# Kernel tuning notes

Measured on AMD Instinct MI355X. Metric: run time of the kernel, lower is better.

## Reference

```python
import jax, jax.numpy as jnp
import numpy as np

N_NODES = 50000
N_EDGES = 1600000
N_GRAPHS = 2048
DIM = 133
EPS = 1e-5


def gcn_conv(x, W, b, row, col, n_nodes):
    # PyG GCNConv: h = x @ W; add self-loops; sym-normalized scatter-add; + b
    h = x @ W  # [N, D]
    loops = jnp.arange(n_nodes, dtype=row.dtype)
    r = jnp.concatenate([row, loops])
    c = jnp.concatenate([col, loops])
    deg = jax.ops.segment_sum(jnp.ones_like(c, dtype=h.dtype), c, num_segments=n_nodes)
    dinv = jnp.where(deg > 0, jax.lax.rsqrt(deg), 0.0)
    norm = dinv[r] * dinv[c]  # [E+N]
    msg = h[r] * norm[:, None]  # gather + scale
    out = jax.ops.segment_sum(msg, c, num_segments=n_nodes)
    return out + b


def batchnorm_eval(x, gamma, beta, rm, rv):
    return (x - rm) * jax.lax.rsqrt(rv + EPS) * gamma + beta


def setup_inputs() -> dict:
    key = jax.random.key(0)
    ks = jax.random.split(key, 8)
    x = jax.random.normal(ks[0], (N_NODES, DIM), dtype=jnp.float32)
    edge_index = jax.random.randint(ks[1], (2, N_EDGES), 0, N_NODES, dtype=jnp.int64)
    batch = jnp.sort(jax.random.randint(ks[2], (N_NODES,), 0, N_GRAPHS, dtype=jnp.int64))
    s = 1.0 / np.sqrt(DIM)
    W1 = jax.random.uniform(ks[3], (DIM, DIM), jnp.float32, -s, s)
    W2 = jax.random.uniform(ks[4], (DIM, DIM), jnp.float32, -s, s)
    b1 = jnp.zeros((DIM,), jnp.float32)
    b2 = jnp.zeros((DIM,), jnp.float32)
    g1 = jnp.ones((DIM,), jnp.float32); beta1 = jnp.zeros((DIM,), jnp.float32)
    rm1 = jax.random.normal(ks[5], (DIM,), jnp.float32) * 0.1
    rv1 = jnp.ones((DIM,), jnp.float32)
    g2 = jnp.ones((DIM,), jnp.float32); beta2 = jnp.zeros((DIM,), jnp.float32)
    rm2 = jax.random.normal(ks[6], (DIM,), jnp.float32) * 0.1
    rv2 = jnp.ones((DIM,), jnp.float32)
    return {"x": x, "edge_index": edge_index, "batch": batch,
            "W1": W1, "b1": b1, "W2": W2, "b2": b2,
            "g1": g1, "beta1": beta1, "rm1": rm1, "rv1": rv1,
            "g2": g2, "beta2": beta2, "rm2": rm2, "rv2": rv2}


def reference(x, edge_index, batch, W1, b1, W2, b2,
              g1, beta1, rm1, rv1, g2, beta2, rm2, rv2):
    row, col = edge_index[0], edge_index[1]
    h = gcn_conv(x, W1, b1, row, col, N_NODES)
    h = jax.nn.relu(h)
    h = batchnorm_eval(h, g1, beta1, rm1, rv1)  # eval-mode BN; dropout is identity in eval
    h = gcn_conv(h, W2, b2, row, col, N_NODES)
    h = jax.nn.relu(h)
    h = batchnorm_eval(h, g2, beta2, rm2, rv2)
    # global mean pool per graph
    sums = jax.ops.segment_sum(h, batch, num_segments=N_GRAPHS)
    cnts = jax.ops.segment_sum(jnp.ones((N_NODES,), h.dtype), batch, num_segments=N_GRAPHS)
    return sums / jnp.maximum(cnts, 1.0)[:, None]
```

## Files before the change

### kernel.cpp

```cpp
#include <hip/hip_runtime.h>

#define N_NODES  50000
#define N_ROWS   50048
#define N_EDGES  1600000
#define N_GRAPHS 2048
#define DIM      133
#define HSTR     136
#define YSTR     160
#define EPSV     1e-5f
#define NRANGE   16
#define RSPAN    3125
#define NSLICE   64
#define BUCKCAP  110000
#define EPB      1563

typedef __attribute__((ext_vector_type(8))) short bf16x8;
typedef __attribute__((ext_vector_type(4))) float f32x4;

__device__ __forceinline__ float blo(unsigned u) { return __uint_as_float(u << 16); }
__device__ __forceinline__ float bhi(unsigned u) { return __uint_as_float(u & 0xFFFF0000u); }
__device__ __forceinline__ unsigned short f2bf(float x) {
    unsigned v = __float_as_uint(x);
    return (unsigned short)((v + 0x7FFFu + ((v >> 16) & 1u)) >> 16);
}
__device__ __forceinline__ unsigned packbf(float a, float b) {
    return (unsigned)f2bf(a) | ((unsigned)f2bf(b) << 16);
}


__global__ __launch_bounds__(256) void k_part(const int* __restrict__ row,
                                              const int* __restrict__ col,
                                              int* __restrict__ bcnt,
                                              unsigned* __restrict__ buckets)
{
    __shared__ int cnt[NRANGE];
    __shared__ int cur[NRANGE];
    int e0 = blockIdx.x * EPB;
    if (threadIdx.x < NRANGE) cnt[threadIdx.x] = 0;
    __syncthreads();
    int e1 = min(e0 + EPB, N_EDGES);
    for (int e = e0 + threadIdx.x; e < e1; e += 256)
        atomicAdd(&cnt[col[e] / RSPAN], 1);
    __syncthreads();
    if (threadIdx.x < NRANGE)
        cur[threadIdx.x] = atomicAdd(&bcnt[threadIdx.x], cnt[threadIdx.x]);
    __syncthreads();
    for (int e = e0 + threadIdx.x; e < e1; e += 256) {
        int c = col[e];
        int r = c / RSPAN;
        int p = atomicAdd(&cur[r], 1);
        buckets[(size_t)r * BUCKCAP + p] =
            ((unsigned)row[e] << 12) | (unsigned)(c - r * RSPAN);
    }
}

__global__ __launch_bounds__(256) void k_count2(const unsigned* __restrict__ buckets,
                                                const int* __restrict__ bcnt,
                                                int* __restrict__ deg2)
{
    __shared__ int hist[RSPAN];
    int r = blockIdx.x & (NRANGE - 1);
    int s = blockIdx.x >> 4;
    int lo = r * RSPAN;
    for (int i = threadIdx.x; i < RSPAN; i += 256) hist[i] = 0;
    __syncthreads();
    int n = bcnt[r];
    int chunk = (n + NSLICE - 1) / NSLICE;
    int e0 = s * chunk, e1 = min(e0 + chunk, n);
    const unsigned* b = buckets + (size_t)r * BUCKCAP;
    for (int e = e0 + threadIdx.x; e < e1; e += 256)
        atomicAdd(&hist[b[e] & 0xFFFu], 1);
    __syncthreads();
    for (int i = threadIdx.x; i < RSPAN; i += 256)
        deg2[(size_t)s * N_NODES + lo + i] = hist[i];
}

__device__ __forceinline__ void w2bf_one(const float* __restrict__ W,
                                         unsigned short* __restrict__ Wbf, int idx)
{
    int j    = idx & 7;
    int lane = (idx >> 3) & 63;
    int kc   = (idx >> 9) % 5;
    int t    = idx / (8 * 64 * 5);
    int k = kc * 32 + (lane >> 4) * 8 + j;
    int n = t * 16 + (lane & 15);
    float v = (k < DIM && n < DIM) ? W[k * DIM + n] : 0.f;
    Wbf[idx] = f2bf(v);
}

__global__ __launch_bounds__(256) void k_setup(const float* __restrict__ W1,
                                               const float* __restrict__ W2,
                                               unsigned short* __restrict__ Wbf1,
                                               unsigned short* __restrict__ Wbf2,
                                               const int* __restrict__ batch,
                                               float* __restrict__ inv_cnt)
{
    int tid = blockIdx.x * 256 + threadIdx.x;
    if (tid < 23040) {
        w2bf_one(W1, Wbf1, tid);
    } else if (tid < 46080) {
        w2bf_one(W2, Wbf2, tid - 23040);
    } else if (tid < 46080 + N_GRAPHS) {
        int g = tid - 46080;
        int a0 = 0, b0 = N_NODES;
        while (a0 < b0) { int m = (a0 + b0) >> 1; if (batch[m] < g) a0 = m + 1; else b0 = m; }
        int a1 = a0, b1 = N_NODES;
        while (a1 < b1) { int m = (a1 + b1) >> 1; if (batch[m] < g + 1) a1 = m + 1; else b1 = m; }
        inv_cnt[g] = 1.0f / (float)max(a1 - a0, 1);
    }
}

__global__ __launch_bounds__(256) void k_scan1(const int* __restrict__ deg2,
                                               float* __restrict__ dinv,
                                               int* __restrict__ offs,
                                               int* __restrict__ bsum)
{
    __shared__ int sd[256];
    int t = threadIdx.x;
    int idx = blockIdx.x * 256 + t;
    int v = 0;
    if (idx < N_NODES) {
        for (int s = 0; s < NSLICE; s++) v += deg2[(size_t)s * N_NODES + idx];
        dinv[idx] = rsqrtf((float)v + 1.0f);
    }
    sd[t] = v; __syncthreads();
    for (int o = 1; o < 256; o <<= 1) {
        int add = (t >= o) ? sd[t - o] : 0;
        __syncthreads();
        sd[t] += add;
        __syncthreads();
    }
    if (idx < N_NODES) offs[idx] = sd[t] - v;
    if (t == 255) bsum[blockIdx.x] = sd[255];
}

__global__ __launch_bounds__(256) void k_scan2(const int* __restrict__ bsum,
                                               int* __restrict__ boff, int nb)
{
    __shared__ int sd[256];
    int t = threadIdx.x;
    int v = (t < nb) ? bsum[t] : 0;
    sd[t] = v; __syncthreads();
    for (int o = 1; o < 256; o <<= 1) {
        int add = (t >= o) ? sd[t - o] : 0;
        __syncthreads();
        sd[t] += add;
        __syncthreads();
    }
    boff[t] = sd[t] - v;
}

__global__ __launch_bounds__(256) void k_scan3C(int* __restrict__ offs,
                                                const int* __restrict__ boff,
                                                int* __restrict__ deg2)
{
    int idx = blockIdx.x * 256 + threadIdx.x;
    if (idx < N_NODES) {
        int off = offs[idx] + boff[blockIdx.x];
        offs[idx] = off;
        int run = off;
        for (int s = 0; s < NSLICE; s++) {
            int d = deg2[(size_t)s * N_NODES + idx];
            deg2[(size_t)s * N_NODES + idx] = run;
            run += d;
        }
    } else if (idx == N_NODES) {
        offs[N_NODES] = N_EDGES;
    }
}

__global__ __launch_bounds__(256) void k_fill2(const unsigned* __restrict__ buckets,
                                               const int* __restrict__ bcnt,
                                               const int* __restrict__ offs2,
                                               unsigned short* __restrict__ csr_src)
{
    __shared__ int cur[RSPAN];
    int r = blockIdx.x & (NRANGE - 1);
    int s = blockIdx.x >> 4;
    int lo = r * RSPAN;
    for (int i = threadIdx.x; i < RSPAN; i += 256)
        cur[i] = offs2[(size_t)s * N_NODES + lo + i];
    __syncthreads();
    int n = bcnt[r];
    int chunk = (n + NSLICE - 1) / NSLICE;
    int e0 = s * chunk, e1 = min(e0 + chunk, n);
    const unsigned* b = buckets + (size_t)r * BUCKCAP;
    for (int e = e0 + threadIdx.x; e < e1; e += 256) {
        unsigned v = b[e];
        int p = atomicAdd(&cur[v & 0xFFFu], 1);
        csr_src[p] = (unsigned short)(v >> 12);
    }
}

__global__ __launch_bounds__(256) void k_x2bf(const float* __restrict__ x,
                                              unsigned* __restrict__ Abf)
{
    int idx = blockIdx.x * 256 + threadIdx.x;
    if (idx >= N_NODES * 80) return;
    int r  = idx / 80;
    int c2 = (idx - r * 80) * 2;
    float a = (c2     < DIM) ? x[(size_t)r * DIM + c2]     : 0.f;
    float b = (c2 + 1 < DIM) ? x[(size_t)r * DIM + c2 + 1] : 0.f;
    Abf[idx] = packbf(a, b);
}

__global__ __launch_bounds__(256) void k_gemm_mfma(const unsigned short* __restrict__ A,
                                                   const unsigned short* __restrict__ Wbf,
                                                   unsigned short* __restrict__ H, int M)
{
    int wave = threadIdx.x >> 6, lane = threadIdx.x & 63;
    int quad = lane >> 4, l16 = lane & 15;
    int m = blockIdx.x * 64 + wave * 16 + l16;

    const bf16x8* Arow = (const bf16x8*)(A + (size_t)m * YSTR);
    const bf16x8* Bq   = (const bf16x8*)Wbf;

    f32x4 acc[9] = {};
#pragma unroll
    for (int kc = 0; kc < 5; kc++) {
        bf16x8 af = Arow[kc * 4 + quad];
#pragma unroll
        for (int t = 0; t < 9; t++) {
            bf16x8 bfr = Bq[(t * 5 + kc) * 64 + lane];
            acc[t] = __builtin_amdgcn_mfma_f32_16x16x32_bf16(af, bfr, acc[t], 0, 0, 0);
        }
    }

    int gr0 = blockIdx.x * 64 + wave * 16 + quad * 4;
#pragma unroll
    for (int t = 0; t < 9; t++) {
        int c = t * 16 + l16;
#pragma unroll
        for (int reg = 0; reg < 4; reg++) {
            int gr = gr0 + reg;
            if (gr < M && c < HSTR) {
                float v = (c < DIM) ? acc[t][reg] : 0.f;
                H[(size_t)gr * HSTR + c] = f2bf(v);
            }
        }
    }
}


template <bool FINAL>
__global__ __launch_bounds__(256) void k_agg(const unsigned short* __restrict__ h,
                                             const int* __restrict__ offs,
                                             const unsigned short* __restrict__ csr_src,
                                             const float* __restrict__ dinv,
                                             const float* __restrict__ bias,
                                             const float* __restrict__ gam,
                                             const float* __restrict__ bet,
                                             const float* __restrict__ rmean,
                                             const float* __restrict__ rvar,
                                             unsigned short* __restrict__ y,
                                             const int* __restrict__ batch,
                                             const float* __restrict__ inv_cnt,
                                             float* __restrict__ outp)
{
    int node = blockIdx.x * 4 + (threadIdx.x >> 6);
    if (node >= N_NODES) return;
    int lane = threadIdx.x & 63;
    int l2 = lane & 3;

    float di = dinv[node];
    const unsigned* hrow = (const unsigned*)(h + (size_t)node * HSTR);
    unsigned p0 = hrow[lane];
    unsigned p1 = hrow[64 + l2];
    float2 a0; a0.x = di * blo(p0); a0.y = di * bhi(p0);
    float2 a1; a1.x = di * blo(p1); a1.y = di * bhi(p1);

    int s0 = offs[node], s1 = offs[node + 1];
    for (int k0 = s0; k0 < s1; k0 += 64) {
        int nk = min(64, s1 - k0);
        int src = 0; float w = 0.f;
        if (lane < nk) {
            src = csr_src[k0 + lane];
            w   = dinv[src];
        }
        int j = 0;
        for (; j + 8 <= nk; j += 8) {
            int   ss[8];
            float wv[8];
#pragma unroll
            for (int u = 0; u < 8; u++) {
                ss[u] = __builtin_amdgcn_readfirstlane(__shfl(src, j + u));
                wv[u] = __shfl(w, j + u);
            }
            unsigned q0[8], q1[8];
#pragma unroll
            for (int u = 0; u < 8; u++) {
                const unsigned* r = (const unsigned*)(h + (size_t)ss[u] * HSTR);
                q0[u] = r[lane];
                q1[u] = r[64 + l2];
            }
#pragma unroll
            for (int u = 0; u < 8; u++) {
                a0.x += wv[u] * blo(q0[u]); a0.y += wv[u] * bhi(q0[u]);
                a1.x += wv[u] * blo(q1[u]); a1.y += wv[u] * bhi(q1[u]);
            }
        }
        for (; j < nk; j++) {
            int   s  = __builtin_amdgcn_readfirstlane(__shfl(src, j));
            float ww = __shfl(w, j);
            const unsigned* hr = (const unsigned*)(h + (size_t)s * HSTR);
            unsigned q0 = hr[lane];
            unsigned q1 = hr[64 + l2];
            a0.x += ww * blo(q0); a0.y += ww * bhi(q0);
            a1.x += ww * blo(q1); a1.y += ww * bhi(q1);
        }
    }

    float ic = 0.f; int bg = 0;
    if (FINAL) { bg = batch[node]; ic = inv_cnt[bg]; }

    {
        int c = 2 * lane;
        float va = di * a0.x + bias[c];
        va = fmaxf(va, 0.f);
        va = (va - rmean[c]) * (gam[c] * rsqrtf(rvar[c] + EPSV)) + bet[c];
        int c1 = c + 1;
        float vb = di * a0.y + bias[c1];
        vb = fmaxf(vb, 0.f);
        vb = (vb - rmean[c1]) * (gam[c1] * rsqrtf(rvar[c1] + EPSV)) + bet[c1];
        if (FINAL) {
            atomicAdd(&outp[(size_t)bg * DIM + c],  va * ic);
            atomicAdd(&outp[(size_t)bg * DIM + c1], vb * ic);
        } else {
            ((unsigned*)(y + (size_t)node * YSTR))[lane] = packbf(va, vb);
        }
    }
    if (lane < 16) {
        float va = 0.f, vb = 0.f;
        if (lane < 4) {
            int c = 128 + 2 * l2;
            if (c < DIM) {
                va = di * a1.x + bias[c];
                va = fmaxf(va, 0.f);
                va = (va - rmean[c]) * (gam[c] * rsqrtf(rvar[c] + EPSV)) + bet[c];
            }
            int c1 = c + 1;
            if (c1 < DIM) {
                vb = di * a1.y + bias[c1];
                vb = fmaxf(vb, 0.f);
                vb = (vb - rmean[c1]) * (gam[c1] * rsqrtf(rvar[c1] + EPSV)) + bet[c1];
            }
            if (FINAL) {
                if (c  < DIM) atomicAdd(&outp[(size_t)bg * DIM + c],  va * ic);
                if (c1 < DIM) atomicAdd(&outp[(size_t)bg * DIM + c1], vb * ic);
            }
        }
        if (!FINAL)
            ((unsigned*)(y + (size_t)node * YSTR))[64 + lane] = packbf(va, vb);
    }
}


extern "C" void kernel_launch(void* const* d_in, const int* in_sizes, int n_in,
                              void* d_out, int out_size, void* d_ws, size_t ws_size,
                              hipStream_t stream)
{
    const float* x   = (const float*)d_in[0];
    const int*   ei  = (const int*)d_in[1];
    const int*   bat = (const int*)d_in[2];
    const float* W1  = (const float*)d_in[3];
    const float* b1  = (const float*)d_in[4];
    const float* W2  = (const float*)d_in[5];
    const float* b2  = (const float*)d_in[6];
    const float* g1  = (const float*)d_in[7];
    const float* be1 = (const float*)d_in[8];
    const float* rm1 = (const float*)d_in[9];
    const float* rv1 = (const float*)d_in[10];
    const float* g2  = (const float*)d_in[11];
    const float* be2 = (const float*)d_in[12];
    const float* rm2 = (const float*)d_in[13];
    const float* rv2 = (const float*)d_in[14];
    float* outp = (float*)d_out;
    char* ws = (char*)d_ws;

    int*   bcnt    = (int*)  (ws + 0);
    int*   offs    = (int*)  (ws + 200000);
    float* dinv    = (float*)(ws + 400016);
    float* inv_cnt = (float*)(ws + 600016);
    int*   bsum    = (int*)  (ws + 608208);
    int*   boff    = (int*)  (ws + 609232);
    unsigned short* csr_src = (unsigned short*)(ws + 610256);
    unsigned short* Wbf1 = (unsigned short*)(ws + 3810256);
    unsigned short* Wbf2 = (unsigned short*)(ws + 3856336);
    unsigned short* Abf  = (unsigned short*)(ws + 3902416);
    unsigned short* Hb   = (unsigned short*)(ws + 19917776);
    unsigned short* Y1   = (unsigned short*)(ws + 33530832);
    unsigned* buckets = (unsigned*)(ws + 19917776);
    int*      deg2    = (int*)    (ws + 26957776);

    hipMemsetAsync(bcnt, 0, 64, stream);
    hipMemsetAsync(d_out, 0, (size_t)out_size * 4, stream);

    const int* row = ei;
    const int* col = ei + N_EDGES;

    int nbl = (N_NODES + 255) / 256;

    k_part  <<<dim3(1024), dim3(256), 0, stream>>>(row, col, bcnt, buckets);
    k_setup <<<dim3(189), dim3(256), 0, stream>>>(W1, W2, Wbf1, Wbf2, bat, inv_cnt);
    k_count2<<<dim3(NSLICE * NRANGE), dim3(256), 0, stream>>>(buckets, bcnt, deg2);
    k_scan1 <<<dim3(nbl), dim3(256), 0, stream>>>(deg2, dinv, offs, bsum);
    k_scan2 <<<dim3(1),   dim3(256), 0, stream>>>(bsum, boff, nbl);
    k_scan3C<<<dim3(nbl), dim3(256), 0, stream>>>(offs, boff, deg2);
    k_fill2 <<<dim3(NSLICE * NRANGE), dim3(256), 0, stream>>>(buckets, bcnt, deg2, csr_src);

    k_x2bf<<<dim3((N_NODES * 80 + 255) / 256), dim3(256), 0, stream>>>(x, (unsigned*)Abf);

    int gbl = N_ROWS / 64;
    k_gemm_mfma<<<dim3(gbl), dim3(256), 0, stream>>>(Abf, Wbf1, Hb, N_NODES);
    k_agg<false><<<dim3(N_NODES / 4), dim3(256), 0, stream>>>(Hb, offs, csr_src, dinv,
                                                              b1, g1, be1, rm1, rv1,
                                                              Y1, nullptr, nullptr, nullptr);
    k_gemm_mfma<<<dim3(gbl), dim3(256), 0, stream>>>(Y1, Wbf2, Hb, N_NODES);
    k_agg<true><<<dim3(N_NODES / 4), dim3(256), 0, stream>>>(Hb, offs, csr_src, dinv,
                                                             b2, g2, be2, rm2, rv2,
                                                             nullptr, bat, inv_cnt, outp);
}
```

Baseline: 357.2 us.

## Pack source index and bf16 weight into CSR records, merge prep kernels

```diff
diff --git a/kernel.cpp b/kernel.cpp
--- a/kernel.cpp
+++ b/kernel.cpp
@@ -88,14 +88,28 @@
     Wbf[idx] = f2bf(v);
 }
 
-__global__ __launch_bounds__(256) void k_setup(const float* __restrict__ W1,
-                                               const float* __restrict__ W2,
-                                               unsigned short* __restrict__ Wbf1,
-                                               unsigned short* __restrict__ Wbf2,
-                                               const int* __restrict__ batch,
-                                               float* __restrict__ inv_cnt)
-{
-    int tid = blockIdx.x * 256 + threadIdx.x;
+#define X2BF_BLOCKS 15625
+
+__global__ __launch_bounds__(256) void k_prep(const float* __restrict__ x,
+                                              unsigned* __restrict__ Abf,
+                                              const float* __restrict__ W1,
+                                              const float* __restrict__ W2,
+                                              unsigned short* __restrict__ Wbf1,
+                                              unsigned short* __restrict__ Wbf2,
+                                              const int* __restrict__ batch,
+                                              float* __restrict__ inv_cnt)
+{
+    if (blockIdx.x < X2BF_BLOCKS) {
+        int idx = blockIdx.x * 256 + threadIdx.x;
+        if (idx >= N_NODES * 80) return;
+        int r  = idx / 80;
+        int c2 = (idx - r * 80) * 2;
+        float a = (c2     < DIM) ? x[(size_t)r * DIM + c2]     : 0.f;
+        float b = (c2 + 1 < DIM) ? x[(size_t)r * DIM + c2 + 1] : 0.f;
+        Abf[idx] = packbf(a, b);
+        return;
+    }
+    int tid = (blockIdx.x - X2BF_BLOCKS) * 256 + threadIdx.x;
     if (tid < 23040) {
         w2bf_one(W1, Wbf1, tid);
     } else if (tid < 46080) {
@@ -172,7 +186,8 @@
 __global__ __launch_bounds__(256) void k_fill2(const unsigned* __restrict__ buckets,
                                                const int* __restrict__ bcnt,
                                                const int* __restrict__ offs2,
-                                               unsigned short* __restrict__ csr_src)
+                                               const float* __restrict__ dinv,
+                                               unsigned* __restrict__ csr)
 {
     __shared__ int cur[RSPAN];
     int r = blockIdx.x & (NRANGE - 1);
@@ -187,21 +202,10 @@
     const unsigned* b = buckets + (size_t)r * BUCKCAP;
     for (int e = e0 + threadIdx.x; e < e1; e += 256) {
         unsigned v = b[e];
+        int src = (int)(v >> 12);
         int p = atomicAdd(&cur[v & 0xFFFu], 1);
-        csr_src[p] = (unsigned short)(v >> 12);
-    }
-}
-
-__global__ __launch_bounds__(256) void k_x2bf(const float* __restrict__ x,
-                                              unsigned* __restrict__ Abf)
-{
-    int idx = blockIdx.x * 256 + threadIdx.x;
-    if (idx >= N_NODES * 80) return;
-    int r  = idx / 80;
-    int c2 = (idx - r * 80) * 2;
-    float a = (c2     < DIM) ? x[(size_t)r * DIM + c2]     : 0.f;
-    float b = (c2 + 1 < DIM) ? x[(size_t)r * DIM + c2 + 1] : 0.f;
-    Abf[idx] = packbf(a, b);
+        csr[p] = ((unsigned)src << 16) | (unsigned)f2bf(dinv[src]);
+    }
 }
 
 __global__ __launch_bounds__(256) void k_gemm_mfma(const unsigned short* __restrict__ A,
@@ -245,7 +249,7 @@
 template <bool FINAL>
 __global__ __launch_bounds__(256) void k_agg(const unsigned short* __restrict__ h,
                                              const int* __restrict__ offs,
-                                             const unsigned short* __restrict__ csr_src,
+                                             const unsigned* __restrict__ csr,
                                              const float* __restrict__ dinv,
                                              const float* __restrict__ bias,
                                              const float* __restrict__ gam,
@@ -257,7 +261,7 @@
                                              const float* __restrict__ inv_cnt,
                                              float* __restrict__ outp)
 {
-    int node = blockIdx.x * 4 + (threadIdx.x >> 6);
+    int node = __builtin_amdgcn_readfirstlane(blockIdx.x * 4 + (threadIdx.x >> 6));
     if (node >= N_NODES) return;
     int lane = threadIdx.x & 63;
     int l2 = lane & 3;
@@ -270,44 +274,33 @@
     float2 a1; a1.x = di * blo(p1); a1.y = di * bhi(p1);
 
     int s0 = offs[node], s1 = offs[node + 1];
-    for (int k0 = s0; k0 < s1; k0 += 64) {
-        int nk = min(64, s1 - k0);
-        int src = 0; float w = 0.f;
-        if (lane < nk) {
-            src = csr_src[k0 + lane];
-            w   = dinv[src];
-        }
-        int j = 0;
-        for (; j + 8 <= nk; j += 8) {
-            int   ss[8];
-            float wv[8];
-#pragma unroll
-            for (int u = 0; u < 8; u++) {
-                ss[u] = __builtin_amdgcn_readfirstlane(__shfl(src, j + u));
-                wv[u] = __shfl(w, j + u);
-            }
-            unsigned q0[8], q1[8];
-#pragma unroll
-            for (int u = 0; u < 8; u++) {
-                const unsigned* r = (const unsigned*)(h + (size_t)ss[u] * HSTR);
-                q0[u] = r[lane];
-                q1[u] = r[64 + l2];
-            }
-#pragma unroll
-            for (int u = 0; u < 8; u++) {
-                a0.x += wv[u] * blo(q0[u]); a0.y += wv[u] * bhi(q0[u]);
-                a1.x += wv[u] * blo(q1[u]); a1.y += wv[u] * bhi(q1[u]);
-            }
-        }
-        for (; j < nk; j++) {
-            int   s  = __builtin_amdgcn_readfirstlane(__shfl(src, j));
-            float ww = __shfl(w, j);
-            const unsigned* hr = (const unsigned*)(h + (size_t)s * HSTR);
-            unsigned q0 = hr[lane];
-            unsigned q1 = hr[64 + l2];
-            a0.x += ww * blo(q0); a0.y += ww * bhi(q0);
-            a1.x += ww * blo(q1); a1.y += ww * bhi(q1);
-        }
+    int e = s0;
+    for (; e + 8 <= s1; e += 8) {
+        unsigned rec[8];
+#pragma unroll
+        for (int u = 0; u < 8; u++) rec[u] = csr[e + u];
+        unsigned q0[8], q1[8];
+#pragma unroll
+        for (int u = 0; u < 8; u++) {
+            const unsigned* hr = (const unsigned*)(h + (size_t)(rec[u] >> 16) * HSTR);
+            q0[u] = hr[lane];
+            q1[u] = hr[64 + l2];
+        }
+#pragma unroll
+        for (int u = 0; u < 8; u++) {
+            float w = __uint_as_float(rec[u] << 16);
+            a0.x += w * blo(q0[u]); a0.y += w * bhi(q0[u]);
+            a1.x += w * blo(q1[u]); a1.y += w * bhi(q1[u]);
+        }
+    }
+    for (; e < s1; e++) {
+        unsigned rec = csr[e];
+        float w = __uint_as_float(rec << 16);
+        const unsigned* hr = (const unsigned*)(h + (size_t)(rec >> 16) * HSTR);
+        unsigned q0 = hr[lane];
+        unsigned q1 = hr[64 + l2];
+        a0.x += w * blo(q0); a0.y += w * bhi(q0);
+        a1.x += w * blo(q1); a1.y += w * bhi(q1);
     }
 
     float ic = 0.f; int bg = 0;
@@ -383,14 +376,14 @@
     float* inv_cnt = (float*)(ws + 600016);
     int*   bsum    = (int*)  (ws + 608208);
     int*   boff    = (int*)  (ws + 609232);
-    unsigned short* csr_src = (unsigned short*)(ws + 610256);
-    unsigned short* Wbf1 = (unsigned short*)(ws + 3810256);
-    unsigned short* Wbf2 = (unsigned short*)(ws + 3856336);
-    unsigned short* Abf  = (unsigned short*)(ws + 3902416);
-    unsigned short* Hb   = (unsigned short*)(ws + 19917776);
-    unsigned short* Y1   = (unsigned short*)(ws + 33530832);
-    unsigned* buckets = (unsigned*)(ws + 19917776);
-    int*      deg2    = (int*)    (ws + 26957776);
+    unsigned* csr  = (unsigned*)(ws + 610256);
+    unsigned short* Wbf1 = (unsigned short*)(ws + 7010256);
+    unsigned short* Wbf2 = (unsigned short*)(ws + 7056336);
+    unsigned short* Abf  = (unsigned short*)(ws + 7102416);
+    unsigned short* Y1   = Abf;
+    unsigned short* Hb   = (unsigned short*)(ws + 23117776);
+    unsigned* buckets = (unsigned*)(ws + 23117776);
+    int*      deg2    = (int*)    (ws + 30157776);
 
     hipMemsetAsync(bcnt, 0, 64, stream);
     hipMemsetAsync(d_out, 0, (size_t)out_size * 4, stream);
@@ -401,22 +394,22 @@
     int nbl = (N_NODES + 255) / 256;
 
     k_part  <<<dim3(1024), dim3(256), 0, stream>>>(row, col, bcnt, buckets);
-    k_setup <<<dim3(189), dim3(256), 0, stream>>>(W1, W2, Wbf1, Wbf2, bat, inv_cnt);
+    k_prep  <<<dim3(X2BF_BLOCKS + 189), dim3(256), 0, stream>>>(x, (unsigned*)Abf,
+                                                                W1, W2, Wbf1, Wbf2,
+                                                                bat, inv_cnt);
     k_count2<<<dim3(NSLICE * NRANGE), dim3(256), 0, stream>>>(buckets, bcnt, deg2);
     k_scan1 <<<dim3(nbl), dim3(256), 0, stream>>>(deg2, dinv, offs, bsum);
     k_scan2 <<<dim3(1),   dim3(256), 0, stream>>>(bsum, boff, nbl);
     k_scan3C<<<dim3(nbl), dim3(256), 0, stream>>>(offs, boff, deg2);
-    k_fill2 <<<dim3(NSLICE * NRANGE), dim3(256), 0, stream>>>(buckets, bcnt, deg2, csr_src);
-
-    k_x2bf<<<dim3((N_NODES * 80 + 255) / 256), dim3(256), 0, stream>>>(x, (unsigned*)Abf);
+    k_fill2 <<<dim3(NSLICE * NRANGE), dim3(256), 0, stream>>>(buckets, bcnt, deg2, dinv, csr);
 
     int gbl = N_ROWS / 64;
     k_gemm_mfma<<<dim3(gbl), dim3(256), 0, stream>>>(Abf, Wbf1, Hb, N_NODES);
-    k_agg<false><<<dim3(N_NODES / 4), dim3(256), 0, stream>>>(Hb, offs, csr_src, dinv,
+    k_agg<false><<<dim3(N_NODES / 4), dim3(256), 0, stream>>>(Hb, offs, csr, dinv,
                                                               b1, g1, be1, rm1, rv1,
                                                               Y1, nullptr, nullptr, nullptr);
     k_gemm_mfma<<<dim3(gbl), dim3(256), 0, stream>>>(Y1, Wbf2, Hb, N_NODES);
-    k_agg<true><<<dim3(N_NODES / 4), dim3(256), 0, stream>>>(Hb, offs, csr_src, dinv,
+    k_agg<true><<<dim3(N_NODES / 4), dim3(256), 0, stream>>>(Hb, offs, csr, dinv,
                                                              b2, g2, be2, rm2, rv2,
                                                              nullptr, bat, inv_cnt, outp);
 }
```

New measurement: 354.7 us (median of 2 runs). No clear change (-0.7%).
